# Kernel tuning notes

Measured on AMD Instinct MI355X. Metric: run time of the kernel, lower is better.

The kernel has to match this reference:

```python
import jax, jax.numpy as jnp
import numpy as np

NUM_HEADS = 16
SLICE_SIZE = 1024
SCALING = SLICE_SIZE ** 0.5  # module divides by sqrt(slice_size), as written


def setup_inputs() -> dict:
    key = jax.random.key(0)
    ks = jax.random.split(key, 9)
    B, S, D = 4, 2048, SLICE_SIZE
    sc = 0.02
    return {
        "x": jax.random.normal(ks[0], (B, S, D), dtype=jnp.float32),
        "Wq": jax.random.normal(ks[1], (D, D), dtype=jnp.float32) * sc,
        "bq": jax.random.normal(ks[2], (D,), dtype=jnp.float32) * sc,
        "Wk": jax.random.normal(ks[3], (D, D), dtype=jnp.float32) * sc,
        "bk": jax.random.normal(ks[4], (D,), dtype=jnp.float32) * sc,
        "Wv": jax.random.normal(ks[5], (D, D), dtype=jnp.float32) * sc,
        "bv": jax.random.normal(ks[6], (D,), dtype=jnp.float32) * sc,
        "Wp": jax.random.normal(ks[7], (D, D), dtype=jnp.float32) * sc,
        "bp": jax.random.normal(ks[8], (D,), dtype=jnp.float32) * sc,
    }


def _split_heads(t):
    # 'b s (h o) -> b h s o'
    b, s, d = t.shape
    return t.reshape(b, s, NUM_HEADS, d // NUM_HEADS).transpose(0, 2, 1, 3)


def reference(x, Wq, bq, Wk, bk, Wv, bv, Wp, bp):
    q = _split_heads(x @ Wq.T + bq)  # [B,H,S,O]
    k = _split_heads(x @ Wk.T + bk)
    v = _split_heads(x @ Wv.T + bv)
    energy = jnp.einsum('bhqo,bhko->bhqk', q, k)  # full score matrix
    attn = jax.nn.softmax(energy / SCALING, axis=-1)
    # Faithful to source: 'b h q k, b h v o -> b h v o' sums attn over (q,k)
    out = jnp.einsum('bhqk,bhvo->bhvo', attn, v)
    b, h, s, o = out.shape
    out = out.transpose(0, 2, 1, 3).reshape(b, s, h * o)  # 'b h v o -> b v (h o)'
    return out @ Wp.T + bp
```

## Files before the change

### kernel.cpp

```cpp
#include <hip/hip_runtime.h>
#include <cstdint>


typedef unsigned short u16;
typedef __bf16 bf16x8 __attribute__((ext_vector_type(8)));
typedef float f32x4 __attribute__((ext_vector_type(4)));

__device__ __forceinline__ u16 f2bf(float f) {
  unsigned int u = __float_as_uint(f);
  u += 0x7fffu + ((u >> 16) & 1u);
  return (u16)(u >> 16);
}

__device__ __forceinline__ void load16(const void* g, void* l) {
  auto gp = (const __attribute__((address_space(1))) unsigned int*)(uintptr_t)g;
  auto lp = (__attribute__((address_space(3))) unsigned int*)(unsigned int)(uintptr_t)l;
  __builtin_amdgcn_global_load_lds(gp, lp, 16, 0, 0);
}

__global__ void k_prep(const float* __restrict__ x, const float* __restrict__ Wv,
                       const float* __restrict__ bv, const float* __restrict__ Wp,
                       const float* __restrict__ bp, u16* __restrict__ xb,
                       u16* __restrict__ wpb, u16* __restrict__ wvtb,
                       float* __restrict__ cv) {
  __shared__ float tile[32][33];
  const int b = blockIdx.x;
  const int tid = threadIdx.x;
  if (b < 9216) {
    const float* src = (b < 8192) ? x : Wp;
    u16* dst = (b < 8192) ? xb : wpb;
    const long base = (long)((b < 8192) ? b : (b - 8192)) * 1024 + tid * 4;
    const float4 v = *(const float4*)(src + base);
    ushort4 o;
    o.x = f2bf(v.x); o.y = f2bf(v.y); o.z = f2bf(v.z); o.w = f2bf(v.w);
    *(ushort4*)(dst + base) = o;
  } else if (b < 10240) {
    const int tb = b - 9216;
    const int bi = (tb & 31) * 32;
    const int bj = (tb >> 5) * 32;
    const int tx = tid & 31;
    const int ty = tid >> 5;
    for (int r = ty; r < 32; r += 8)
      tile[r][tx] = Wv[(long)(bj + r) * 1024 + bi + tx];
    __syncthreads();
    for (int r = ty; r < 32; r += 8)
      wvtb[(long)(bi + r) * 1024 + bj + tx] = f2bf(tile[tx][r]);
  } else {
    const int row = (b - 10240) * 4 + (tid >> 6);
    const int lane = tid & 63;
    const float* w = Wp + (long)row * 1024;
    float s = 0.f;
    for (int j = lane; j < 1024; j += 64) s += w[j] * bv[j];
    for (int off = 32; off; off >>= 1) s += __shfl_down(s, off, 64);
    if (lane == 0) cv[row] = 2048.f * s + bp[row];
  }
}

__global__ void k_reduce(const float* __restrict__ p, u16* __restrict__ dst) {
  const long i = (long)(blockIdx.x * 256 + threadIdx.x) * 4;
  const float4 a = *(const float4*)(p + i);
  const float4 b = *(const float4*)(p + 1048576 + i);
  const float4 c = *(const float4*)(p + 2097152 + i);
  const float4 d = *(const float4*)(p + 3145728 + i);
  ushort4 o;
  o.x = f2bf((a.x + b.x + c.x + d.x) * 2048.f);
  o.y = f2bf((a.y + b.y + c.y + d.y) * 2048.f);
  o.z = f2bf((a.z + b.z + c.z + d.z) * 2048.f);
  o.w = f2bf((a.w + b.w + c.w + d.w) * 2048.f);
  *(ushort4*)(dst + i) = o;
}

template <int MODE, int NB>
__global__ __launch_bounds__(256, 3) void k_gemm(
    const u16* __restrict__ A, const u16* __restrict__ B, float* __restrict__ Out,
    const float* __restrict__ bias, int M, int N, int K) {
  __shared__ u16 As[64 * 32];
  __shared__ u16 Bs[256 * 32];

  const int tid = threadIdx.x;
  const int lane = tid & 63;
  const int wv = tid >> 6;
  const int waveN = wv << 6;
  const int l15 = lane & 15;
  const int quad = lane >> 4;

  long bm, bn;
  int kBeg, kEnd;
  if constexpr (MODE == 0) {
    const int id = blockIdx.x;
    const int xcd = id & 7;
    const int j = id >> 3;
    const int mPerXcd = M / 64 / 8;
    bm = (long)(xcd * mPerXcd + j / NB) * 64;
    bn = (long)(j % NB) * 256;
    kBeg = 0; kEnd = K;
  } else {
    bm = (long)blockIdx.x * 64;
    bn = (long)blockIdx.y * 256;
    const int kChunk = K / gridDim.z;
    kBeg = blockIdx.z * kChunk;
    kEnd = kBeg + kChunk;
  }

  const int srow = tid >> 2;
  const int scol = (tid & 3) << 3;
  const u16* Ag = A + (bm + srow) * K + scol;
  const u16* Bg = B + (bn + srow) * K + scol;
  u16* As0 = As + wv * 512;
  u16* Bs0 = Bs + wv * 512;

  const f32x4 zero = {0.f, 0.f, 0.f, 0.f};
  f32x4 acc[4][4];
#pragma unroll
  for (int i = 0; i < 4; ++i)
#pragma unroll
    for (int j = 0; j < 4; ++j) acc[i][j] = zero;

  for (int k0 = kBeg; k0 < kEnd; k0 += 32) {
    __syncthreads();
    load16(Ag + k0, As0);
#pragma unroll
    for (int r = 0; r < 4; ++r)
      load16(Bg + (long)r * 64 * K + k0, Bs0 + r * 2048);
    __syncthreads();

    bf16x8 af[4], bg[4];
#pragma unroll
    for (int t = 0; t < 4; ++t) {
      af[t] = *(const bf16x8*)(As + (t * 16 + l15) * 32 + quad * 8);
      bg[t] = *(const bf16x8*)(Bs + (waveN + t * 16 + l15) * 32 + quad * 8);
    }
#pragma unroll
    for (int i = 0; i < 4; ++i)
#pragma unroll
      for (int j = 0; j < 4; ++j)
        acc[i][j] = __builtin_amdgcn_mfma_f32_16x16x32_bf16(af[i], bg[j], acc[i][j], 0, 0, 0);
  }

  float* outp = (MODE == 1) ? Out + (long)blockIdx.z * M * N : Out;
#pragma unroll
  for (int i = 0; i < 4; ++i) {
    const long gm = bm + i * 16 + quad * 4;
#pragma unroll
    for (int j = 0; j < 4; ++j) {
      const long gn = bn + waveN + j * 16 + l15;
      const float bb = (MODE == 0) ? bias[gn] : 0.f;
#pragma unroll
      for (int r = 0; r < 4; ++r)
        outp[(gm + r) * N + gn] = acc[i][j][r] + bb;
    }
  }
}

extern "C" void kernel_launch(void* const* d_in, const int* in_sizes, int n_in,
                              void* d_out, int out_size, void* d_ws, size_t ws_size,
                              hipStream_t stream) {
  const float* x  = (const float*)d_in[0];
  const float* Wv = (const float*)d_in[5];
  const float* bv = (const float*)d_in[6];
  const float* Wp = (const float*)d_in[7];
  const float* bp = (const float*)d_in[8];

  char* ws = (char*)d_ws;
  u16* xb    = (u16*)(ws);
  u16* wpb   = (u16*)(ws + (16u << 20));
  u16* wvtb  = (u16*)(ws + (18u << 20));
  u16* m2b   = (u16*)(ws + (20u << 20));
  float* cv  = (float*)(ws + (22u << 20));
  float* m2f = (float*)(ws + (22u << 20) + 4096);

  k_prep<<<10496, 256, 0, stream>>>(x, Wv, bv, Wp, bp, xb, wpb, wvtb, cv);

  k_gemm<1, 4><<<dim3(16, 4, 4), 256, 0, stream>>>(wpb, wvtb, m2f, nullptr,
                                                   1024, 1024, 1024);
  k_reduce<<<1024, 256, 0, stream>>>(m2f, m2b);

  k_gemm<0, 4><<<512, 256, 0, stream>>>(xb, m2b, (float*)d_out, cv,
                                        8192, 1024, 1024);
}
```

Before: 153.5 us.

## Switch GEMM to 128x128 tiles with K=128 stages and XOR-swizzled LDS

Changes the GEMM block tile from 64x256 with K-step 32 to a square 128x128 tile with K-step 128. The four waves now form a 2x2 grid, and the LDS layout uses an XOR swizzle on 16-byte chunks to avoid bank conflicts on the fragment reads. The intent is better operand reuse and fewer barrier round trips per unit of MFMA work. In exchange, shared memory grows to 64KB per block and launch bounds drop to 2 blocks per CU, which lowers occupancy with no double buffering to hide load latency.

```diff
diff --git a/kernel.cpp b/kernel.cpp
--- a/kernel.cpp
+++ b/kernel.cpp
@@ -70,17 +70,18 @@
   *(ushort4*)(dst + i) = o;
 }
 
-template <int MODE, int NB>
-__global__ __launch_bounds__(256, 3) void k_gemm(
+template <int MODE>
+__global__ __launch_bounds__(256, 2) void k_gemm(
     const u16* __restrict__ A, const u16* __restrict__ B, float* __restrict__ Out,
     const float* __restrict__ bias, int M, int N, int K) {
-  __shared__ u16 As[64 * 32];
-  __shared__ u16 Bs[256 * 32];
+  __shared__ u16 As[128 * 128];
+  __shared__ u16 Bs[128 * 128];
 
   const int tid = threadIdx.x;
   const int lane = tid & 63;
   const int wv = tid >> 6;
-  const int waveN = wv << 6;
+  const int waveM = (wv & 1) << 6;
+  const int waveN = (wv >> 1) << 6;
   const int l15 = lane & 15;
   const int quad = lane >> 4;
 
@@ -90,24 +91,26 @@
     const int id = blockIdx.x;
     const int xcd = id & 7;
     const int j = id >> 3;
-    const int mPerXcd = M / 64 / 8;
-    bm = (long)(xcd * mPerXcd + j / NB) * 64;
-    bn = (long)(j % NB) * 256;
+    const int nb = N >> 7;
+    const int mPerXcd = M / 128 / 8;
+    bm = (long)(xcd * mPerXcd + j / nb) * 128;
+    bn = (long)(j % nb) * 128;
     kBeg = 0; kEnd = K;
   } else {
-    bm = (long)blockIdx.x * 64;
-    bn = (long)blockIdx.y * 256;
+    bm = (long)blockIdx.x * 128;
+    bn = (long)blockIdx.y * 128;
     const int kChunk = K / gridDim.z;
     kBeg = blockIdx.z * kChunk;
     kEnd = kBeg + kChunk;
   }
 
-  const int srow = tid >> 2;
-  const int scol = (tid & 3) << 3;
-  const u16* Ag = A + (bm + srow) * K + scol;
-  const u16* Bg = B + (bn + srow) * K + scol;
-  u16* As0 = As + wv * 512;
-  u16* Bs0 = Bs + wv * 512;
+  const int rr = (wv << 2) + (lane >> 4);
+  const int s15 = lane & 15;
+  const int kc = s15 ^ (rr & 7);
+  const u16* Ag = A + (bm + rr) * (long)K + kc * 8;
+  const u16* Bg = B + (bn + rr) * (long)K + kc * 8;
+  u16* Asw = As + (wv << 9);
+  u16* Bsw = Bs + (wv << 9);
 
   const f32x4 zero = {0.f, 0.f, 0.f, 0.f};
   f32x4 acc[4][4];
@@ -116,31 +119,37 @@
 #pragma unroll
     for (int j = 0; j < 4; ++j) acc[i][j] = zero;
 
-  for (int k0 = kBeg; k0 < kEnd; k0 += 32) {
+  for (int k0 = kBeg; k0 < kEnd; k0 += 128) {
     __syncthreads();
-    load16(Ag + k0, As0);
 #pragma unroll
-    for (int r = 0; r < 4; ++r)
-      load16(Bg + (long)r * 64 * K + k0, Bs0 + r * 2048);
+    for (int r = 0; r < 8; ++r)
+      load16(Ag + (long)(r * 16) * K + k0, Asw + r * 2048);
+#pragma unroll
+    for (int r = 0; r < 8; ++r)
+      load16(Bg + (long)(r * 16) * K + k0, Bsw + r * 2048);
     __syncthreads();
 
-    bf16x8 af[4], bg[4];
 #pragma unroll
-    for (int t = 0; t < 4; ++t) {
-      af[t] = *(const bf16x8*)(As + (t * 16 + l15) * 32 + quad * 8);
-      bg[t] = *(const bf16x8*)(Bs + (waveN + t * 16 + l15) * 32 + quad * 8);
+    for (int kk = 0; kk < 4; ++kk) {
+      const int swz = ((kk << 2) + quad) ^ (l15 & 7);
+      bf16x8 af[4], bg[4];
+#pragma unroll
+      for (int t = 0; t < 4; ++t) {
+        af[t] = *(const bf16x8*)(As + (waveM + t * 16 + l15) * 128 + swz * 8);
+        bg[t] = *(const bf16x8*)(Bs + (waveN + t * 16 + l15) * 128 + swz * 8);
+      }
+#pragma unroll
+      for (int i = 0; i < 4; ++i)
+#pragma unroll
+        for (int j = 0; j < 4; ++j)
+          acc[i][j] = __builtin_amdgcn_mfma_f32_16x16x32_bf16(af[i], bg[j], acc[i][j], 0, 0, 0);
     }
-#pragma unroll
-    for (int i = 0; i < 4; ++i)
-#pragma unroll
-      for (int j = 0; j < 4; ++j)
-        acc[i][j] = __builtin_amdgcn_mfma_f32_16x16x32_bf16(af[i], bg[j], acc[i][j], 0, 0, 0);
   }
 
   float* outp = (MODE == 1) ? Out + (long)blockIdx.z * M * N : Out;
 #pragma unroll
   for (int i = 0; i < 4; ++i) {
-    const long gm = bm + i * 16 + quad * 4;
+    const long gm = bm + waveM + i * 16 + quad * 4;
 #pragma unroll
     for (int j = 0; j < 4; ++j) {
       const long gn = bn + waveN + j * 16 + l15;
@@ -171,10 +180,10 @@
 
   k_prep<<<10496, 256, 0, stream>>>(x, Wv, bv, Wp, bp, xb, wpb, wvtb, cv);
 
-  k_gemm<1, 4><<<dim3(16, 4, 4), 256, 0, stream>>>(wpb, wvtb, m2f, nullptr,
-                                                   1024, 1024, 1024);
+  k_gemm<1><<<dim3(8, 8, 4), 256, 0, stream>>>(wpb, wvtb, m2f, nullptr,
+                                               1024, 1024, 1024);
   k_reduce<<<1024, 256, 0, stream>>>(m2f, m2b);
 
-  k_gemm<0, 4><<<512, 256, 0, stream>>>(xb, m2b, (float*)d_out, cv,
-                                        8192, 1024, 1024);
+  k_gemm<0><<<512, 256, 0, stream>>>(xb, m2b, (float*)d_out, cv,
+                                     8192, 1024, 1024);
 }
```

Result: faster. 140.7 us (-8.3%).
